# Kernel optimization log

Hardware: AMD Instinct MI355X
Metric: run time of the kernel (lower is better)

## Reference

```python
import jax, jax.numpy as jnp
import numpy as np

B, N, D, H = 8, 1024, 1024, 16
HD = D // H  # head_size = 64


def setup_inputs() -> dict:
    key = jax.random.key(0)
    k0, k1, k2, k3, k4 = jax.random.split(key, 5)
    scale = 1.0 / np.sqrt(D)
    return {
        "x": jax.random.normal(k0, (B, N, D), dtype=jnp.float32),
        "Wqkv": jax.random.normal(k1, (D, 3 * D), dtype=jnp.float32) * scale,
        "bqkv": jnp.zeros((3 * D,), dtype=jnp.float32),
        "Wo": jax.random.normal(k2, (D, D), dtype=jnp.float32) * scale,
        "bo": jnp.zeros((D,), dtype=jnp.float32),
    }


def reference(x, Wqkv, bqkv, Wo, bo):
    # Fused QKV projection: [B, N, 3D]
    qkv = jnp.einsum("bnd,de->bne", x, Wqkv) + bqkv
    q, k, v = jnp.split(qkv, 3, axis=-1)

    def split_heads(t):  # [B, N, D] -> [B, H, N, HD]
        return t.reshape(B, N, H, HD).transpose(0, 2, 1, 3)

    q, k, v = split_heads(q), split_heads(k), split_heads(v)

    # Scaled dot-product attention (no mask, dropout=0)
    scores = jnp.einsum("bhqd,bhkd->bhqk", q, k) / jnp.sqrt(jnp.float32(HD))
    alpha = jax.nn.softmax(scores, axis=-1)
    ctx = jnp.einsum("bhqk,bhkd->bhqd", alpha, v)  # [B, H, N, HD]

    ctx = ctx.transpose(0, 2, 1, 3).reshape(B, N, D)
    out = jnp.einsum("bnd,de->bne", ctx, Wo) + bo
    return out
```

## Files before the change

kernel.cpp:

```cpp
#include <hip/hip_runtime.h>
#include <cstdint>
#include <cstddef>

typedef _Float16 half_t;
typedef __attribute__((ext_vector_type(4))) _Float16 half4v;
typedef __attribute__((ext_vector_type(8))) _Float16 half8v;
typedef __attribute__((ext_vector_type(4))) float float4v;
typedef __attribute__((ext_vector_type(16))) float float16v;
typedef __attribute__((ext_vector_type(4))) unsigned uint4v;
typedef __attribute__((ext_vector_type(2))) int int2v;

typedef __attribute__((address_space(1))) const void gv_t;
typedef __attribute__((address_space(3))) void lv_t;

__device__ __forceinline__ void lds_cp16(const void* g, void* l) {
  __builtin_amdgcn_global_load_lds((gv_t*)g, (lv_t*)l, 16, 0, 0);
}

__device__ __forceinline__ unsigned pkh(float a, float b) {
  return __builtin_bit_cast(unsigned, __builtin_amdgcn_cvt_pkrtz(a, b));
}

__global__ __launch_bounds__(256) void k_cvt(const float* __restrict__ in,
                                             half_t* __restrict__ out) {
  int i = blockIdx.x * 256 + threadIdx.x;
  float4 v = ((const float4*)in)[i];
  half4v h = {(half_t)v.x, (half_t)v.y, (half_t)v.z, (half_t)v.w};
  ((half4v*)out)[i] = h;
}

__global__ __launch_bounds__(256) void k_tcvt(const float* __restrict__ in,
                                              half_t* __restrict__ out, int R, int C) {
  __shared__ float t[32][33];
  int c0 = blockIdx.x * 32, r0 = blockIdx.y * 32;
  int tc = threadIdx.x & 31, tr = threadIdx.x >> 5;
#pragma unroll
  for (int i = 0; i < 4; i++)
    t[tr + i * 8][tc] = in[(size_t)(r0 + tr + i * 8) * C + c0 + tc];
  __syncthreads();
#pragma unroll
  for (int i = 0; i < 4; i++)
    out[(size_t)(c0 + tr + i * 8) * R + r0 + tc] = (half_t)t[tc][tr + i * 8];
}

template <int EPI>
__global__ __launch_bounds__(256) void k_gemm(
    const half_t* __restrict__ A, const half_t* __restrict__ Bt,
    const float* __restrict__ bias, float* __restrict__ Cout,
    half_t* __restrict__ Qo, half_t* __restrict__ Ko, half_t* __restrict__ Vo,
    int M, int N, int K) {
  __shared__ half_t As[4][128 * 32];
  __shared__ half_t Bs[4][128 * 32];
  const int tid = threadIdx.x;
  const int lane = tid & 63;
  const int w = tid >> 6;
  const int xcd = blockIdx.x & 7;
  const int l = blockIdx.x >> 3;
  const int nc = l >> 6, r = l & 63;
  const int m0 = (xcd * 8 + (r >> 3)) * 128;
  const int n0 = (nc * 8 + (r & 7)) * 128;
  const int wr = w >> 1, wc = w & 1;

  const int c0 = w * 2, c1 = c0 + 1;
  const int srow = lane >> 2;
  const int sr0 = c0 * 16 + srow;
  const int sr1 = c1 * 16 + srow;
  const int scol = ((lane & 3) ^ ((lane >> 3) & 3)) * 8;

  const half_t* Ag0 = A + (size_t)(m0 + sr0) * K + scol;
  const half_t* Ag1 = A + (size_t)(m0 + sr1) * K + scol;
  const half_t* Bg0 = Bt + (size_t)(n0 + sr0) * K + scol;
  const half_t* Bg1 = Bt + (size_t)(n0 + sr1) * K + scol;

  float4v acc[4][4] = {};

  const int fr = lane & 15;
  const int fg = lane >> 4;
  const int cswz = (fg ^ ((fr >> 1) & 3)) * 8;
  const int aoff = (wr * 64 + fr) * 32 + cswz;
  const int boff = (wc * 64 + fr) * 32 + cswz;

  const int NT = K >> 5;
#pragma unroll
  for (int p = 0; p < 2; ++p) {
    const int kn = p * 32;
    lds_cp16(Ag0 + kn, &As[p][c0 * 512]);
    lds_cp16(Ag1 + kn, &As[p][c1 * 512]);
    lds_cp16(Bg0 + kn, &Bs[p][c0 * 512]);
    lds_cp16(Bg1 + kn, &Bs[p][c1 * 512]);
  }

  for (int t = 0; t < NT; t++) {
    if (t + 2 < NT) {
      const int nb = (t + 2) & 3;
      const int kn = (t + 2) * 32;
      lds_cp16(Ag0 + kn, &As[nb][c0 * 512]);
      lds_cp16(Ag1 + kn, &As[nb][c1 * 512]);
      lds_cp16(Bg0 + kn, &Bs[nb][c0 * 512]);
      lds_cp16(Bg1 + kn, &Bs[nb][c1 * 512]);
    }
    if (t + 2 < NT)
      asm volatile("s_waitcnt vmcnt(8)" ::: "memory");
    else if (t + 1 < NT)
      asm volatile("s_waitcnt vmcnt(4)" ::: "memory");
    else
      asm volatile("s_waitcnt vmcnt(0)" ::: "memory");
    __builtin_amdgcn_s_barrier();
    __builtin_amdgcn_sched_barrier(0);

    const int cb = t & 3;
    half8v a[4], b[4];
#pragma unroll
    for (int m = 0; m < 4; m++) a[m] = *(const half8v*)(&As[cb][aoff + m * 512]);
#pragma unroll
    for (int n = 0; n < 4; n++) b[n] = *(const half8v*)(&Bs[cb][boff + n * 512]);
    __builtin_amdgcn_s_setprio(1);
#pragma unroll
    for (int m = 0; m < 4; m++)
#pragma unroll
      for (int n = 0; n < 4; n++)
        acc[m][n] = __builtin_amdgcn_mfma_f32_16x16x32_f16(a[m], b[n], acc[m][n], 0, 0, 0);
    __builtin_amdgcn_s_setprio(0);
  }

  const int rq = (lane >> 4) * 4;
  const int cc = lane & 15;
  if constexpr (EPI == 0) {
#pragma unroll
    for (int n = 0; n < 4; n++) {
      int e = n0 + wc * 64 + n * 16 + cc;
      float bv = bias[e];
      int which = e >> 10, h = (e >> 6) & 15, hd = e & 63;
#pragma unroll
      for (int m = 0; m < 4; m++) {
        int rowb = m0 + wr * 64 + m * 16 + rq;
#pragma unroll
        for (int r2 = 0; r2 < 4; r2++) {
          int row = rowb + r2;
          int b_ = row >> 10, tok = row & 1023;
          half_t hv = (half_t)(acc[m][n][r2] + bv);
          size_t bh = (size_t)(b_ * 16 + h);
          if (which == 0)
            Qo[(bh * 1024 + tok) * 64 + hd] = hv;
          else if (which == 1)
            Ko[(bh * 1024 + tok) * 64 + hd] = hv;
          else
            Vo[(bh * 64 + hd) * 1024 + tok] = hv;
        }
      }
    }
  } else {
#pragma unroll
    for (int n = 0; n < 4; n++) {
      int e = n0 + wc * 64 + n * 16 + cc;
      float bv = bias[e];
#pragma unroll
      for (int m = 0; m < 4; m++) {
        int rowb = m0 + wr * 64 + m * 16 + rq;
#pragma unroll
        for (int r2 = 0; r2 < 4; r2++)
          Cout[(size_t)(rowb + r2) * N + e] = acc[m][n][r2] + bv;
      }
    }
  }
}

__global__ __launch_bounds__(512, 4) void k_attn(const half_t* __restrict__ Qh,
                                                 const half_t* __restrict__ Kh,
                                                 const half_t* __restrict__ Vt,
                                                 half_t* __restrict__ ctx) {
  __shared__ alignas(16) half_t Ks[2][64 * 64];
  __shared__ alignas(16) half_t Vs[2][64 * 64];
  const int lane = threadIdx.x & 63;
  const int w = threadIdx.x >> 6;
  const int ql = lane & 31, hi = lane >> 5;
  const int xcd = blockIdx.x & 7, loc = blockIdx.x >> 3;
  const int bh = xcd * 16 + (loc >> 2), qb = loc & 3;
  const int b_ = bh >> 4, h = bh & 15;
  const int q0 = qb * 256 + w * 32;

  const half_t* Qp = Qh + (size_t)bh * (1024 * 64);
  const half_t* Kp = Kh + (size_t)bh * (1024 * 64);
  const half_t* Vp = Vt + (size_t)bh * (64 * 1024);

  half8v qf[4];
#pragma unroll
  for (int c = 0; c < 4; c++) {
    half8v tq = *(const half8v*)(Qp + (size_t)(q0 + ql) * 64 + c * 16 + hi * 8);
    qf[c] = tq * (_Float16)0.125f;
  }

  const int G = w * 64 + lane;
  const int rS = G >> 3;
  const int gS = (G & 7) ^ (rS & 7);

  float16v co[2] = {};
  float mr = -1e30f, ssum = 0.f;

  lds_cp16(Kp + (size_t)rS * 64 + gS * 8, &Ks[0][w * 512]);
  lds_cp16(Vp + (size_t)rS * 1024 + 0 + gS * 8, &Vs[0][w * 512]);
  __syncthreads();

  int cur = 0;
  for (int t = 0; t < 16; t++) {
    if (t < 15) {
      const int kn = (t + 1) * 64;
      lds_cp16(Kp + (size_t)(kn + rS) * 64 + gS * 8, &Ks[cur ^ 1][w * 512]);
      lds_cp16(Vp + (size_t)rS * 1024 + kn + gS * 8, &Vs[cur ^ 1][w * 512]);
    }

    float16v sacc[2] = {};
    __builtin_amdgcn_s_setprio(1);
#pragma unroll
    for (int c = 0; c < 4; c++)
#pragma unroll
      for (int s = 0; s < 2; s++) {
        int row = s * 32 + ql;
        half8v kf = *(const half8v*)(&Ks[cur][row * 64 + (((2 * c + hi) ^ (row & 7)) * 8)]);
        sacc[s] = __builtin_amdgcn_mfma_f32_32x32x16_f16(kf, qf[c], sacc[s], 0, 0, 0);
      }
    __builtin_amdgcn_s_setprio(0);

    float mx = -1e30f;
#pragma unroll
    for (int s = 0; s < 2; s++)
#pragma unroll
      for (int i = 0; i < 16; i++) mx = fmaxf(mx, sacc[s][i]);
    mx = fmaxf(mx, __shfl_xor(mx, 32, 64));
    if (mx > mr + 8.f) {
      float fac = __expf(mr - mx);
      mr = mx;
      ssum *= fac;
#pragma unroll
      for (int dd = 0; dd < 2; dd++)
#pragma unroll
        for (int i = 0; i < 16; i++) co[dd][i] *= fac;
    }
    float rsum = 0.f;
#pragma unroll
    for (int s = 0; s < 2; s++)
#pragma unroll
      for (int i = 0; i < 16; i++) {
        float e = __expf(sacc[s][i] - mr);
        sacc[s][i] = e;
        rsum += e;
      }
    rsum += __shfl_xor(rsum, 32, 64);
    ssum += rsum;

#pragma unroll
    for (int kc = 0; kc < 4; kc++) {
      const int s = kc >> 1, o = (kc & 1) * 8;
      unsigned dA0 = pkh(sacc[s][o + 0], sacc[s][o + 1]);
      unsigned dA1 = pkh(sacc[s][o + 2], sacc[s][o + 3]);
      unsigned dB0 = pkh(sacc[s][o + 4], sacc[s][o + 5]);
      unsigned dB1 = pkh(sacc[s][o + 6], sacc[s][o + 7]);
      int2v r0 = __builtin_amdgcn_permlane32_swap((int)dA0, (int)dB0, false, false);
      int2v r1 = __builtin_amdgcn_permlane32_swap((int)dA1, (int)dB1, false, false);
      uint4v pw = {(unsigned)r0.x, (unsigned)r1.x, (unsigned)r0.y, (unsigned)r1.y};
      half8v pf = __builtin_bit_cast(half8v, pw);
      __builtin_amdgcn_s_setprio(1);
#pragma unroll
      for (int dd = 0; dd < 2; dd++) {
        int row = dd * 32 + ql;
        half8v vf = *(const half8v*)(&Vs[cur][row * 64 + (((2 * kc + hi) ^ (row & 7)) * 8)]);
        co[dd] = __builtin_amdgcn_mfma_f32_32x32x16_f16(vf, pf, co[dd], 0, 0, 0);
      }
      __builtin_amdgcn_s_setprio(0);
    }
    __syncthreads();
    cur ^= 1;
  }

  float rinv = 1.0f / ssum;
  half_t* outp = ctx + ((size_t)(b_ * 1024 + q0 + ql) * 1024 + h * 64);
#pragma unroll
  for (int dd = 0; dd < 2; dd++)
#pragma unroll
    for (int g = 0; g < 4; g++) {
      int d0 = dd * 32 + g * 8 + hi * 4;
      unsigned p0 = pkh(co[dd][g * 4 + 0] * rinv, co[dd][g * 4 + 1] * rinv);
      unsigned p1 = pkh(co[dd][g * 4 + 2] * rinv, co[dd][g * 4 + 3] * rinv);
      *(unsigned*)(outp + d0) = p0;
      *(unsigned*)(outp + d0 + 2) = p1;
    }
}

extern "C" void kernel_launch(void* const* d_in, const int* in_sizes, int n_in,
                              void* d_out, int out_size, void* d_ws, size_t ws_size,
                              hipStream_t stream) {
  const float* x = (const float*)d_in[0];
  const float* Wqkv = (const float*)d_in[1];
  const float* bqkv = (const float*)d_in[2];
  const float* Wo = (const float*)d_in[3];
  const float* bo = (const float*)d_in[4];
  float* out = (float*)d_out;
  char* ws = (char*)d_ws;

  const size_t NEED = 75497472;
  if (ws_size < NEED) return;
  half_t* xh = (half_t*)(ws);
  half_t* wqkvT = (half_t*)(ws + 16777216);
  half_t* woT = (half_t*)(ws + 23068672);
  half_t* Qh = (half_t*)(ws + 25165824);
  half_t* Kh = (half_t*)(ws + 41943040);
  half_t* Vt = (half_t*)(ws + 58720256);
  half_t* ctxh = xh;

  k_cvt<<<8192, 256, 0, stream>>>(x, xh);
  k_tcvt<<<dim3(96, 32), 256, 0, stream>>>(Wqkv, wqkvT, 1024, 3072);
  k_tcvt<<<dim3(32, 32), 256, 0, stream>>>(Wo, woT, 1024, 1024);
  k_gemm<0><<<1536, 256, 0, stream>>>(xh, wqkvT, bqkv, nullptr, Qh, Kh, Vt,
                                      8192, 3072, 1024);
  k_attn<<<512, 512, 0, stream>>>(Qh, Kh, Vt, ctxh);
  k_gemm<1><<<512, 256, 0, stream>>>(ctxh, woT, bo, out, nullptr, nullptr, nullptr,
                                     8192, 1024, 1024);
}
```

Before: 176.6 us.

## Replace QKV GEMM with 256x256-tile 8-wave kernel and interleaved staging

The QKV projection GEMM gets its own kernel: 256x256 output tiles per 512-thread block, a K-step of 64, and double-buffered swizzled LDS. Global-to-LDS copies for the next stages are interleaved between four MFMA quadrant phases, with explicit barriers, waitcnt and setprio. The goal is higher arithmetic intensity per LDS byte and better overlap of memory with compute. The cost is 128KB of LDS, heavy register use from 32 accumulators per lane, and only 384 blocks across the CUs, so tail effects and occupancy may hurt.

```diff
diff --git a/kernel.cpp b/kernel.cpp
--- a/kernel.cpp
+++ b/kernel.cpp
@@ -43,12 +43,182 @@
     out[(size_t)(c0 + tr + i * 8) * R + r0 + tc] = (half_t)t[tc][tr + i * 8];
 }
 
-template <int EPI>
-__global__ __launch_bounds__(256) void k_gemm(
+__global__ __launch_bounds__(512, 2) void k_gemm_qkv(
     const half_t* __restrict__ A, const half_t* __restrict__ Bt,
-    const float* __restrict__ bias, float* __restrict__ Cout,
-    half_t* __restrict__ Qo, half_t* __restrict__ Ko, half_t* __restrict__ Vo,
-    int M, int N, int K) {
+    const float* __restrict__ bias,
+    half_t* __restrict__ Qo, half_t* __restrict__ Ko, half_t* __restrict__ Vo) {
+  __shared__ half_t S[2][2][256 * 64];
+  const int tid = threadIdx.x;
+  const int lane = tid & 63;
+  const int w = tid >> 6;
+  const int wr = w >> 2, wc = w & 3;
+  const int fr = lane & 15, fg = lane >> 4;
+
+  const int bid = blockIdx.x;
+  const int xcd = bid & 7, l = bid >> 3;
+  const int mi = xcd * 4 + (l & 3);
+  const int ni = (l >> 4) * 4 + ((l >> 2) & 3);
+  const int m0 = mi * 256, n0 = ni * 256;
+
+  const int G0 = tid, G1 = 512 + tid;
+  const int ar0 = G0 >> 3, ar1 = G1 >> 3;
+  const int sg0 = (G0 & 7) ^ (ar0 & 7), sg1 = (G1 & 7) ^ (ar1 & 7);
+  const size_t aof0 = (size_t)(m0 + ar0) * 1024 + sg0 * 8;
+  const size_t aof1 = (size_t)(m0 + ar1) * 1024 + sg1 * 8;
+  const size_t bof0 = (size_t)(n0 + ar0) * 1024 + sg0 * 8;
+  const size_t bof1 = (size_t)(n0 + ar1) * 1024 + sg1 * 8;
+  const int d0 = G0 * 8, d1 = G1 * 8;
+
+#define STG_A(hf, T, bf)                                                     \
+  do {                                                                       \
+    lds_cp16(A + aof0 + (hf) * 131072 + (T) * 64, &S[bf][0][(hf)*8192 + d0]); \
+    lds_cp16(A + aof1 + (hf) * 131072 + (T) * 64, &S[bf][0][(hf)*8192 + d1]); \
+  } while (0)
+#define STG_B(hf, T, bf)                                                      \
+  do {                                                                        \
+    lds_cp16(Bt + bof0 + (hf) * 131072 + (T) * 64, &S[bf][1][(hf)*8192 + d0]); \
+    lds_cp16(Bt + bof1 + (hf) * 131072 + (T) * 64, &S[bf][1][(hf)*8192 + d1]); \
+  } while (0)
+
+  const int so0 = ((0 << 2) | fg) ^ (fr & 7);
+  const int so1 = ((1 << 2) | fg) ^ (fr & 7);
+
+  float4v acc[8][4] = {};
+  half8v a[8][2], b[2][2];
+
+  STG_A(0, 0, 0); STG_A(1, 0, 0); STG_B(0, 0, 0); STG_B(1, 0, 0);
+  STG_A(0, 1, 1); STG_A(1, 1, 1); STG_B(0, 1, 1);
+  asm volatile("s_waitcnt vmcnt(6)" ::: "memory");
+  __builtin_amdgcn_s_barrier();
+
+  for (int T = 0; T < 16; ++T) {
+    const int cb = T & 1, nb = cb ^ 1;
+#pragma unroll
+    for (int m = 0; m < 4; ++m) {
+      const int row = (wr * 128 + m * 16 + fr) * 64;
+      a[m][0] = *(const half8v*)(&S[cb][0][row + so0 * 8]);
+      a[m][1] = *(const half8v*)(&S[cb][0][row + so1 * 8]);
+    }
+#pragma unroll
+    for (int n = 0; n < 2; ++n) {
+      const int row = (wc * 64 + n * 16 + fr) * 64;
+      b[n][0] = *(const half8v*)(&S[cb][1][row + so0 * 8]);
+      b[n][1] = *(const half8v*)(&S[cb][1][row + so1 * 8]);
+    }
+    if (T < 15) STG_B(1, T + 1, nb);
+    __builtin_amdgcn_s_barrier();
+    asm volatile("s_waitcnt lgkmcnt(0)" ::: "memory");
+    __builtin_amdgcn_sched_barrier(0);
+    __builtin_amdgcn_s_setprio(1);
+#pragma unroll
+    for (int kk = 0; kk < 2; ++kk)
+#pragma unroll
+      for (int m = 0; m < 4; ++m)
+#pragma unroll
+        for (int n = 0; n < 2; ++n)
+          acc[m][n] = __builtin_amdgcn_mfma_f32_16x16x32_f16(a[m][kk], b[n][kk],
+                                                             acc[m][n], 0, 0, 0);
+    __builtin_amdgcn_s_setprio(0);
+    __builtin_amdgcn_s_barrier();
+
+#pragma unroll
+    for (int m = 4; m < 8; ++m) {
+      const int row = (wr * 128 + m * 16 + fr) * 64;
+      a[m][0] = *(const half8v*)(&S[cb][0][row + so0 * 8]);
+      a[m][1] = *(const half8v*)(&S[cb][0][row + so1 * 8]);
+    }
+    __builtin_amdgcn_s_barrier();
+    asm volatile("s_waitcnt lgkmcnt(0)" ::: "memory");
+    __builtin_amdgcn_sched_barrier(0);
+    __builtin_amdgcn_s_setprio(1);
+#pragma unroll
+    for (int kk = 0; kk < 2; ++kk)
+#pragma unroll
+      for (int m = 4; m < 8; ++m)
+#pragma unroll
+        for (int n = 0; n < 2; ++n)
+          acc[m][n] = __builtin_amdgcn_mfma_f32_16x16x32_f16(a[m][kk], b[n][kk],
+                                                             acc[m][n], 0, 0, 0);
+    __builtin_amdgcn_s_setprio(0);
+    __builtin_amdgcn_s_barrier();
+
+#pragma unroll
+    for (int n = 0; n < 2; ++n) {
+      const int row = (wc * 64 + 32 + n * 16 + fr) * 64;
+      b[n][0] = *(const half8v*)(&S[cb][1][row + so0 * 8]);
+      b[n][1] = *(const half8v*)(&S[cb][1][row + so1 * 8]);
+    }
+    if (T < 14) STG_A(0, T + 2, cb);
+    __builtin_amdgcn_s_barrier();
+    asm volatile("s_waitcnt lgkmcnt(0)" ::: "memory");
+    __builtin_amdgcn_sched_barrier(0);
+    __builtin_amdgcn_s_setprio(1);
+#pragma unroll
+    for (int kk = 0; kk < 2; ++kk)
+#pragma unroll
+      for (int m = 0; m < 4; ++m)
+#pragma unroll
+        for (int n = 0; n < 2; ++n)
+          acc[m][n + 2] = __builtin_amdgcn_mfma_f32_16x16x32_f16(
+              a[m][kk], b[n][kk], acc[m][n + 2], 0, 0, 0);
+    __builtin_amdgcn_s_setprio(0);
+    __builtin_amdgcn_s_barrier();
+
+    if (T < 14) {
+      STG_A(1, T + 2, cb);
+      STG_B(0, T + 2, cb);
+    }
+    if (T == 14)
+      asm volatile("s_waitcnt vmcnt(0)" ::: "memory");
+    else if (T < 14)
+      asm volatile("s_waitcnt vmcnt(6)" ::: "memory");
+    __builtin_amdgcn_s_barrier();
+    __builtin_amdgcn_sched_barrier(0);
+    __builtin_amdgcn_s_setprio(1);
+#pragma unroll
+    for (int kk = 0; kk < 2; ++kk)
+#pragma unroll
+      for (int m = 4; m < 8; ++m)
+#pragma unroll
+        for (int n = 0; n < 2; ++n)
+          acc[m][n + 2] = __builtin_amdgcn_mfma_f32_16x16x32_f16(
+              a[m][kk], b[n][kk], acc[m][n + 2], 0, 0, 0);
+    __builtin_amdgcn_s_setprio(0);
+    __builtin_amdgcn_s_barrier();
+  }
+#undef STG_A
+#undef STG_B
+
+  const int rq = (lane >> 4) * 4;
+  const int cc = lane & 15;
+#pragma unroll
+  for (int n = 0; n < 4; ++n) {
+    const int e = n0 + wc * 64 + n * 16 + cc;
+    const float bv = bias[e];
+    const int which = e >> 10, h = (e >> 6) & 15, hd = e & 63;
+#pragma unroll
+    for (int m = 0; m < 8; ++m) {
+      const int rowb = m0 + wr * 128 + m * 16 + rq;
+#pragma unroll
+      for (int r2 = 0; r2 < 4; ++r2) {
+        const int row = rowb + r2;
+        const int b_ = row >> 10, tok = row & 1023;
+        const half_t hv = (half_t)(acc[m][n][r2] + bv);
+        const size_t bh = (size_t)(b_ * 16 + h);
+        if (which == 0)
+          Qo[(bh * 1024 + tok) * 64 + hd] = hv;
+        else if (which == 1)
+          Ko[(bh * 1024 + tok) * 64 + hd] = hv;
+        else
+          Vo[(bh * 64 + hd) * 1024 + tok] = hv;
+      }
+    }
+  }
+}
+
+__global__ __launch_bounds__(256) void k_gemm_o(
+    const half_t* __restrict__ A, const half_t* __restrict__ Bt,
+    const float* __restrict__ bias, float* __restrict__ Cout, int N, int K) {
   __shared__ half_t As[4][128 * 32];
   __shared__ half_t Bs[4][128 * 32];
   const int tid = threadIdx.x;
@@ -125,42 +295,16 @@
 
   const int rq = (lane >> 4) * 4;
   const int cc = lane & 15;
-  if constexpr (EPI == 0) {
-#pragma unroll
-    for (int n = 0; n < 4; n++) {
-      int e = n0 + wc * 64 + n * 16 + cc;
-      float bv = bias[e];
-      int which = e >> 10, h = (e >> 6) & 15, hd = e & 63;
-#pragma unroll
-      for (int m = 0; m < 4; m++) {
-        int rowb = m0 + wr * 64 + m * 16 + rq;
-#pragma unroll
-        for (int r2 = 0; r2 < 4; r2++) {
-          int row = rowb + r2;
-          int b_ = row >> 10, tok = row & 1023;
-          half_t hv = (half_t)(acc[m][n][r2] + bv);
-          size_t bh = (size_t)(b_ * 16 + h);
-          if (which == 0)
-            Qo[(bh * 1024 + tok) * 64 + hd] = hv;
-          else if (which == 1)
-            Ko[(bh * 1024 + tok) * 64 + hd] = hv;
-          else
-            Vo[(bh * 64 + hd) * 1024 + tok] = hv;
-        }
-      }
-    }
-  } else {
-#pragma unroll
-    for (int n = 0; n < 4; n++) {
-      int e = n0 + wc * 64 + n * 16 + cc;
-      float bv = bias[e];
-#pragma unroll
-      for (int m = 0; m < 4; m++) {
-        int rowb = m0 + wr * 64 + m * 16 + rq;
-#pragma unroll
-        for (int r2 = 0; r2 < 4; r2++)
-          Cout[(size_t)(rowb + r2) * N + e] = acc[m][n][r2] + bv;
-      }
+#pragma unroll
+  for (int n = 0; n < 4; n++) {
+    int e = n0 + wc * 64 + n * 16 + cc;
+    float bv = bias[e];
+#pragma unroll
+    for (int m = 0; m < 4; m++) {
+      int rowb = m0 + wr * 64 + m * 16 + rq;
+#pragma unroll
+      for (int r2 = 0; r2 < 4; r2++)
+        Cout[(size_t)(rowb + r2) * N + e] = acc[m][n][r2] + bv;
     }
   }
 }
@@ -310,9 +454,7 @@
   k_cvt<<<8192, 256, 0, stream>>>(x, xh);
   k_tcvt<<<dim3(96, 32), 256, 0, stream>>>(Wqkv, wqkvT, 1024, 3072);
   k_tcvt<<<dim3(32, 32), 256, 0, stream>>>(Wo, woT, 1024, 1024);
-  k_gemm<0><<<1536, 256, 0, stream>>>(xh, wqkvT, bqkv, nullptr, Qh, Kh, Vt,
-                                      8192, 3072, 1024);
+  k_gemm_qkv<<<384, 512, 0, stream>>>(xh, wqkvT, bqkv, Qh, Kh, Vt);
   k_attn<<<512, 512, 0, stream>>>(Qh, Kh, Vt, ctxh);
-  k_gemm<1><<<512, 256, 0, stream>>>(ctxh, woT, bo, out, nullptr, nullptr, nullptr,
-                                     8192, 1024, 1024);
-}
+  k_gemm_o<<<512, 256, 0, stream>>>(ctxh, woT, bo, out, 1024, 1024);
+}
```

Result: slower. 192.5 us (+9.0%).
